# Kernel tuning notes

Measured on AMD Instinct MI355X. Metric: run time of the kernel, lower is better.

Reference implementation:

```python
import jax, jax.numpy as jnp
import numpy as np

NUM_CATEGORIES = 16
INPUT_DIM = 1024
HIDDEN_DIM = 4096
BATCH = 64
SEQ = 256


def setup_inputs() -> dict:
    key = jax.random.key(0)
    k1, k2, k3 = jax.random.split(key, 3)
    x = jax.random.normal(k1, (BATCH, SEQ, INPUT_DIM), dtype=jnp.float32)
    cat_ids = jax.random.randint(k2, (BATCH,), 0, NUM_CATEGORIES, dtype=jnp.int64)
    W = 0.02 * jax.random.normal(k3, (NUM_CATEGORIES, INPUT_DIM, HIDDEN_DIM), dtype=jnp.float32)
    b = jnp.zeros((NUM_CATEGORIES, HIDDEN_DIM), dtype=jnp.float32)
    return {"x": x, "cat_ids": cat_ids, "W": W, "b": b}


def reference(x, cat_ids, W, b):
    # Gather per-sample expert weights then batched matmul, matching torch.bmm semantics.
    selected_W = W[cat_ids]            # [B, input_dim, hidden_dim]
    selected_b = b[cat_ids]            # [B, hidden_dim]
    out = jnp.einsum('bsi,bih->bsh', x, selected_W) + selected_b[:, None, :]
    return out
```

## Files before the change

kernel.cpp:

```cpp
#include <hip/hip_runtime.h>
#include <hip/hip_bf16.h>
#include <stdint.h>

#define BATCH 64
#define SEQ   256
#define KDIM  1024
#define NDIM  4096
#define NCAT  16

#define BM 128
#define BN 128
#define BK 64
#define MT (SEQ/BM)
#define NT (NDIM/BN)
#define TILES_PER_BATCH (MT*NT)
#define NBLOCKS (BATCH*TILES_PER_BATCH)

typedef __attribute__((ext_vector_type(4))) float f32x4;
typedef __attribute__((ext_vector_type(2))) unsigned int u32x2;
typedef __attribute__((ext_vector_type(4))) unsigned int u32x4;
typedef __attribute__((ext_vector_type(8))) short bf16x8;

__device__ __forceinline__ unsigned short f2bf(float f) {
  __hip_bfloat16 h = __float2bfloat16(f);
  return __builtin_bit_cast(unsigned short, h);
}
__device__ __forceinline__ unsigned pack2(float lo, float hi) {
  return (unsigned)f2bf(lo) | ((unsigned)f2bf(hi) << 16);
}

__device__ __forceinline__ void gload16(const void* g, void* l) {
  __builtin_amdgcn_global_load_lds(
      (const __attribute__((address_space(1))) unsigned int*)g,
      (__attribute__((address_space(3))) unsigned int*)l, 16, 0, 0);
}

__global__ void cvt_x_kernel(const float* __restrict__ x,
                             unsigned short* __restrict__ xb, int n8) {
  int i = blockIdx.x * blockDim.x + threadIdx.x;
  const int stride = gridDim.x * blockDim.x;
  for (; i < n8; i += stride) {
    f32x4 a = ((const f32x4*)x)[2 * i];
    f32x4 b = ((const f32x4*)x)[2 * i + 1];
    u32x4 q;
    q[0] = pack2(a[0], a[1]); q[1] = pack2(a[2], a[3]);
    q[2] = pack2(b[0], b[1]); q[3] = pack2(b[2], b[3]);
    ((u32x4*)xb)[i] = q;
  }
}

__global__ void cvt_w_kernel(const float* __restrict__ W,
                             unsigned short* __restrict__ Wt) {
  __shared__ float ls[64][65];
  const int bid = blockIdx.x;
  const int cat = bid >> 10;
  const int rem = bid & 1023;
  const int kt  = rem >> 6;
  const int ntl = rem & 63;
  const int tid = threadIdx.x;

  const float* src = W + (size_t)cat * KDIM * NDIM + (size_t)(kt * 64) * NDIM + ntl * 64;
  const int kl = tid >> 4;
  const int nl = (tid & 15) * 4;
#pragma unroll
  for (int i = 0; i < 4; ++i) {
    f32x4 v = *(const f32x4*)(src + (size_t)(kl + i * 16) * NDIM + nl);
    ls[kl + i * 16][nl + 0] = v[0];
    ls[kl + i * 16][nl + 1] = v[1];
    ls[kl + i * 16][nl + 2] = v[2];
    ls[kl + i * 16][nl + 3] = v[3];
  }
  __syncthreads();
  const int n  = tid >> 2;
  const int k2 = (tid & 3) * 16;
  u32x4 q0, q1;
#pragma unroll
  for (int j = 0; j < 4; ++j) q0[j] = pack2(ls[k2 + 2 * j][n],     ls[k2 + 2 * j + 1][n]);
#pragma unroll
  for (int j = 0; j < 4; ++j) q1[j] = pack2(ls[k2 + 8 + 2 * j][n], ls[k2 + 9 + 2 * j][n]);
  unsigned short* dst = Wt + (size_t)cat * NDIM * KDIM + (size_t)(ntl * 64 + n) * KDIM + kt * 64 + k2;
  *(u32x4*)dst       = q0;
  *(u32x4*)(dst + 8) = q1;
}

__global__ __launch_bounds__(256, 4)
void csl_gemm(const unsigned short* __restrict__ xb,
              const unsigned short* __restrict__ Wt,
              const int*   __restrict__ cat_ids,
              const float* __restrict__ bias,
              float* __restrict__ out)
{
  __shared__ __align__(16) unsigned char sA[BM * BK * 2];
  __shared__ __align__(16) unsigned char sB[BN * BK * 2];
  __shared__ int s_cat[BATCH];

  const int tid  = threadIdx.x;
  const int lane = tid & 63;
  const int wid  = tid >> 6;

  if (tid < BATCH) s_cat[tid] = cat_ids[tid];
  __syncthreads();

  const int bid  = (int)blockIdx.x;
  const int t_id = (bid & 7) * (NBLOCKS / 8) + (bid >> 3);

  const int myc = s_cat[lane];
  int c = 0, base = 0, cc = 0;
  unsigned long long mask = 0ULL;
  for (c = 0; c < NCAT; ++c) {
    mask = __ballot(myc == c);
    cc = __popcll(mask);
    int sz = cc * TILES_PER_BATCH;
    if (t_id < base + sz) break;
    base += sz;
  }
  if (c >= NCAT) return;
  const int idx    = t_id - base;
  const int per_nt = cc * MT;
  const int nt     = idx / per_nt;
  const int r      = idx % per_nt;
  const int want   = r >> 1;
  const int mt     = r & 1;
  unsigned long long mm = mask;
  for (int i = 0; i < want; ++i) mm &= (mm - 1);
  const int batch = __ffsll((long long)mm) - 1;
  const int cat   = c;

  const int m0 = mt * BM;
  const int n0 = nt * BN;

  const size_t xa = ((size_t)batch * SEQ + m0) * KDIM;
  const size_t wa = ((size_t)cat * NDIM + n0) * KDIM;

  const int srow = tid >> 3;
  const int skq  = tid & 7;
  const unsigned ldsb = (unsigned)(wid * 1024);

  f32x4 acc[4][4] = {};
  const int wr   = (wid >> 1) * 64;
  const int wc   = (wid & 1) * 64;
  const int mcol = lane & 15;
  const int kq16 = (lane >> 4) * 16;

  for (int kt = 0; kt < KDIM / BK; ++kt) {
    const int k0 = kt * BK;
    __syncthreads();
#pragma unroll
    for (int s = 0; s < 4; ++s) {
      const unsigned short* gp = xb + xa + (size_t)(s * 32 + srow) * KDIM + (k0 + skq * 8);
      gload16(gp, sA + s * 4096 + ldsb);
    }
#pragma unroll
    for (int s = 0; s < 4; ++s) {
      const unsigned short* gp = Wt + wa + (size_t)(s * 32 + srow) * KDIM + (k0 + skq * 8);
      gload16(gp, sB + s * 4096 + ldsb);
    }
    __syncthreads();
#pragma unroll
    for (int kk = 0; kk < 2; ++kk) {
      const int kb = kk * 64 + kq16;
      bf16x8 af[4], bfr[4];
#pragma unroll
      for (int mi = 0; mi < 4; ++mi)
        af[mi] = *(const bf16x8*)(sA + (unsigned)((wr + mi * 16 + mcol) * 128 + kb));
#pragma unroll
      for (int ni = 0; ni < 4; ++ni)
        bfr[ni] = *(const bf16x8*)(sB + (unsigned)((wc + ni * 16 + mcol) * 128 + kb));
#pragma unroll
      for (int mi = 0; mi < 4; ++mi)
#pragma unroll
        for (int ni = 0; ni < 4; ++ni)
          acc[mi][ni] = __builtin_amdgcn_mfma_f32_16x16x32_bf16(af[mi], bfr[ni], acc[mi][ni], 0, 0, 0);
    }
  }

  const int col_l = lane & 15;
  const int row_l = (lane >> 4) * 4;
#pragma unroll
  for (int mi = 0; mi < 4; ++mi) {
#pragma unroll
    for (int ni = 0; ni < 4; ++ni) {
      int gr = m0 + wr + mi * 16 + row_l;
      int gc = n0 + wc + ni * 16 + col_l;
      float bvl = bias[(size_t)cat * NDIM + gc];
      f32x4 v = acc[mi][ni];
      size_t o = ((size_t)batch * SEQ + gr) * NDIM + gc;
      out[o]            = v[0] + bvl;
      out[o + NDIM]     = v[1] + bvl;
      out[o + 2 * NDIM] = v[2] + bvl;
      out[o + 3 * NDIM] = v[3] + bvl;
    }
  }
}

__global__ __launch_bounds__(256, 2)
void csl_fallback(const float* __restrict__ x,
                  const int*   __restrict__ cat_ids,
                  const float* __restrict__ W,
                  const float* __restrict__ bias,
                  float* __restrict__ out)
{
  __shared__ __align__(16) unsigned char sA[BM * BK * 2];
  __shared__ __align__(16) unsigned char sB[BN * BK * 2];
  __shared__ int s_cat[BATCH];

  const int tid  = threadIdx.x;
  const int lane = tid & 63;
  const int wid  = tid >> 6;

  if (tid < BATCH) s_cat[tid] = cat_ids[tid];
  __syncthreads();

  const int myc = s_cat[lane];
  int t_id = (int)blockIdx.x;
  int c = 0, base = 0, cc = 0;
  unsigned long long mask = 0ULL;
  for (c = 0; c < NCAT; ++c) {
    mask = __ballot(myc == c);
    cc = __popcll(mask);
    int sz = cc * TILES_PER_BATCH;
    if (t_id < base + sz) break;
    base += sz;
  }
  if (c >= NCAT) return;
  const int idx    = t_id - base;
  const int per_nt = cc * MT;
  const int nt     = idx / per_nt;
  const int r      = idx % per_nt;
  const int want   = r >> 1;
  const int mt     = r & 1;
  unsigned long long mm = mask;
  for (int i = 0; i < want; ++i) mm &= (mm - 1);
  const int batch = __ffsll((long long)mm) - 1;
  const int cat   = c;

  const int m0 = mt * BM;
  const int n0 = nt * BN;

  const size_t x_base = ((size_t)batch * SEQ + m0) * KDIM;
  const size_t w_base = (size_t)cat * KDIM * NDIM + n0;

  f32x4 acc[4][4] = {};
  const int wr = (wid >> 1) * 64;
  const int wc = (wid & 1) * 64;

  for (int kt = 0; kt < KDIM / BK; ++kt) {
    const int k0 = kt * BK;
    f32x4 av[4][2];
#pragma unroll
    for (int s = 0; s < 4; ++s) {
      int seg  = tid + s * 256;
      int arow = seg >> 3;
      int ak   = (seg & 7) << 3;
      const float* gp = x + x_base + (size_t)arow * KDIM + (size_t)(k0 + ak);
      av[s][0] = *(const f32x4*)gp;
      av[s][1] = *(const f32x4*)(gp + 4);
    }
    f32x4 bv[2][4];
#pragma unroll
    for (int s = 0; s < 2; ++s) {
      int u  = tid + s * 256;
      int nq = u & 31;
      int kq = u >> 5;
      const float* gp = W + w_base + (size_t)(k0 + kq * 4) * NDIM + (size_t)(nq * 4);
#pragma unroll
      for (int rr = 0; rr < 4; ++rr)
        bv[s][rr] = *(const f32x4*)(gp + (size_t)rr * NDIM);
    }
    __syncthreads();
#pragma unroll
    for (int s = 0; s < 4; ++s) {
      int seg  = tid + s * 256;
      int arow = seg >> 3;
      int akb  = (seg & 7) << 4;
      unsigned byte = (unsigned)(arow * (BK * 2)) + ((unsigned)akb ^ (((unsigned)arow & 7u) << 4));
      u32x4 q;
      q[0] = pack2(av[s][0][0], av[s][0][1]);
      q[1] = pack2(av[s][0][2], av[s][0][3]);
      q[2] = pack2(av[s][1][0], av[s][1][1]);
      q[3] = pack2(av[s][1][2], av[s][1][3]);
      *(u32x4*)(sA + byte) = q;
    }
#pragma unroll
    for (int s = 0; s < 2; ++s) {
      int u  = tid + s * 256;
      int nq = u & 31;
      int kq = u >> 5;
      unsigned swz = ((unsigned)nq & 7u) << 4;
#pragma unroll
      for (int i = 0; i < 4; ++i) {
        int n = nq * 4 + i;
        unsigned byte = (unsigned)(n * (BK * 2)) + (((unsigned)(kq * 8)) ^ swz);
        u32x2 d;
        d[0] = pack2(bv[s][0][i], bv[s][1][i]);
        d[1] = pack2(bv[s][2][i], bv[s][3][i]);
        *(u32x2*)(sB + byte) = d;
      }
    }
    __syncthreads();
#pragma unroll
    for (int kk = 0; kk < 2; ++kk) {
      const int kb = kk * 64 + ((lane >> 4) << 4);
      bf16x8 af[4], bfr[4];
#pragma unroll
      for (int mi = 0; mi < 4; ++mi) {
        int row = wr + mi * 16 + (lane & 15);
        unsigned byte = (unsigned)(row * (BK * 2)) + ((unsigned)kb ^ (((unsigned)row & 7u) << 4));
        af[mi] = *(const bf16x8*)(sA + byte);
      }
#pragma unroll
      for (int ni = 0; ni < 4; ++ni) {
        int n = wc + ni * 16 + (lane & 15);
        unsigned byte = (unsigned)(n * (BK * 2)) + ((unsigned)kb ^ ((((unsigned)n >> 2) & 7u) << 4));
        bfr[ni] = *(const bf16x8*)(sB + byte);
      }
#pragma unroll
      for (int mi = 0; mi < 4; ++mi)
#pragma unroll
        for (int ni = 0; ni < 4; ++ni)
          acc[mi][ni] = __builtin_amdgcn_mfma_f32_16x16x32_bf16(af[mi], bfr[ni], acc[mi][ni], 0, 0, 0);
    }
  }

  const int col_l = lane & 15;
  const int row_l = (lane >> 4) * 4;
#pragma unroll
  for (int mi = 0; mi < 4; ++mi) {
#pragma unroll
    for (int ni = 0; ni < 4; ++ni) {
      int gr = m0 + wr + mi * 16 + row_l;
      int gc = n0 + wc + ni * 16 + col_l;
      float bvl = bias[(size_t)cat * NDIM + gc];
      f32x4 v = acc[mi][ni];
      size_t o = ((size_t)batch * SEQ + gr) * NDIM + gc;
      out[o]            = v[0] + bvl;
      out[o + NDIM]     = v[1] + bvl;
      out[o + 2 * NDIM] = v[2] + bvl;
      out[o + 3 * NDIM] = v[3] + bvl;
    }
  }
}

extern "C" void kernel_launch(void* const* d_in, const int* in_sizes, int n_in,
                              void* d_out, int out_size, void* d_ws, size_t ws_size,
                              hipStream_t stream) {
  const float* x       = (const float*)d_in[0];
  const int*   cat_ids = (const int*)d_in[1];
  const float* W       = (const float*)d_in[2];
  const float* bias    = (const float*)d_in[3];
  float*       out     = (float*)d_out;
  (void)in_sizes; (void)n_in; (void)out_size;

  const size_t wt_elems = (size_t)NCAT * NDIM * KDIM;
  const size_t xb_elems = (size_t)BATCH * SEQ * KDIM;
  const size_t need = (wt_elems + xb_elems) * sizeof(unsigned short);

  if (ws_size >= need) {
    unsigned short* Wt = (unsigned short*)d_ws;
    unsigned short* xb = Wt + wt_elems;
    hipLaunchKernelGGL(cvt_x_kernel, dim3(2048), dim3(256), 0, stream,
                       x, xb, (int)(xb_elems / 8));
    hipLaunchKernelGGL(cvt_w_kernel, dim3(NCAT * (KDIM / 64) * (NDIM / 64)), dim3(256), 0, stream,
                       W, Wt);
    hipLaunchKernelGGL(csl_gemm, dim3(NBLOCKS), dim3(256), 0, stream,
                       xb, Wt, cat_ids, bias, out);
  } else {
    hipLaunchKernelGGL(csl_fallback, dim3(NBLOCKS), dim3(256), 0, stream,
                       x, cat_ids, W, bias, out);
  }
}
```

Baseline: 299.8 us.

## Use 256x256 tiles with double-buffered pre-swizzled LDS pipeline in grouped GEMM

The main GEMM moves from 128x128 tiles with 256 threads to 256x256 tiles with 512 threads. It uses a 128KB double-buffered LDS pipeline that prefetches the next K-tiles while the current one is computed, with explicit barriers, waitcnts and setprio around the MFMA phases. The conversion kernels now write x and W as bf16 tiles already swizzled in the LDS image, so direct global-to-LDS loads avoid bank conflicts and need only contiguous copies. The aim is to raise arithmetic intensity and hide load latency. The cost is fewer blocks (1024), higher register pressure from 32 accumulators, and a more fragile hand-scheduled sync pattern.

```diff
diff --git a/kernel.cpp b/kernel.cpp
--- a/kernel.cpp
+++ b/kernel.cpp
@@ -8,16 +8,14 @@
 #define NDIM  4096
 #define NCAT  16
 
-#define BM 128
-#define BN 128
+#define BM 256
+#define BN 256
 #define BK 64
-#define MT (SEQ/BM)
-#define NT (NDIM/BN)
-#define TILES_PER_BATCH (MT*NT)
-#define NBLOCKS (BATCH*TILES_PER_BATCH)
+#define NT_G (NDIM/BN)
+#define KT_G (KDIM/BK)
+#define GEMM_BLOCKS (BATCH*NT_G)
 
 typedef __attribute__((ext_vector_type(4))) float f32x4;
-typedef __attribute__((ext_vector_type(2))) unsigned int u32x2;
 typedef __attribute__((ext_vector_type(4))) unsigned int u32x4;
 typedef __attribute__((ext_vector_type(8))) short bf16x8;
 
@@ -28,29 +26,37 @@
 __device__ __forceinline__ unsigned pack2(float lo, float hi) {
   return (unsigned)f2bf(lo) | ((unsigned)f2bf(hi) << 16);
 }
-
 __device__ __forceinline__ void gload16(const void* g, void* l) {
   __builtin_amdgcn_global_load_lds(
       (const __attribute__((address_space(1))) unsigned int*)g,
       (__attribute__((address_space(3))) unsigned int*)l, 16, 0, 0);
 }
 
+
 __global__ void cvt_x_kernel(const float* __restrict__ x,
-                             unsigned short* __restrict__ xb, int n8) {
-  int i = blockIdx.x * blockDim.x + threadIdx.x;
-  const int stride = gridDim.x * blockDim.x;
-  for (; i < n8; i += stride) {
-    f32x4 a = ((const f32x4*)x)[2 * i];
-    f32x4 b = ((const f32x4*)x)[2 * i + 1];
-    u32x4 q;
-    q[0] = pack2(a[0], a[1]); q[1] = pack2(a[2], a[3]);
-    q[2] = pack2(b[0], b[1]); q[3] = pack2(b[2], b[3]);
-    ((u32x4*)xb)[i] = q;
-  }
+                             unsigned char* __restrict__ xb_t) {
+  int g = blockIdx.x * 256 + threadIdx.x;
+  const int row = g >> 7;
+  const int c   = g & 127;
+  const int b   = row >> 8;
+  const int s   = row & 255;
+  const int kt  = c >> 3;
+  const int ck  = c & 7;
+  const int h   = s >> 7;
+  const int r   = s & 127;
+  const float* src = x + (size_t)row * KDIM + c * 8;
+  f32x4 a = *(const f32x4*)src;
+  f32x4 d = *(const f32x4*)(src + 4);
+  u32x4 q;
+  q[0] = pack2(a[0], a[1]); q[1] = pack2(a[2], a[3]);
+  q[2] = pack2(d[0], d[1]); q[3] = pack2(d[2], d[3]);
+  unsigned off = (unsigned)(((b * 16 + kt) * 2 + h) * 16384)
+               + (unsigned)(r * 128) + (((unsigned)(ck * 16)) ^ (((unsigned)r & 7u) << 4));
+  *(u32x4*)(xb_t + off) = q;
 }
 
 __global__ void cvt_w_kernel(const float* __restrict__ W,
-                             unsigned short* __restrict__ Wt) {
+                             unsigned char* __restrict__ Wt) {
   __shared__ float ls[64][65];
   const int bid = blockIdx.x;
   const int cat = bid >> 10;
@@ -78,31 +84,39 @@
   for (int j = 0; j < 4; ++j) q0[j] = pack2(ls[k2 + 2 * j][n],     ls[k2 + 2 * j + 1][n]);
 #pragma unroll
   for (int j = 0; j < 4; ++j) q1[j] = pack2(ls[k2 + 8 + 2 * j][n], ls[k2 + 9 + 2 * j][n]);
-  unsigned short* dst = Wt + (size_t)cat * NDIM * KDIM + (size_t)(ntl * 64 + n) * KDIM + kt * 64 + k2;
-  *(u32x4*)dst       = q0;
-  *(u32x4*)(dst + 8) = q1;
-}
-
-__global__ __launch_bounds__(256, 4)
-void csl_gemm(const unsigned short* __restrict__ xb,
-              const unsigned short* __restrict__ Wt,
+
+  const int nt   = ntl >> 2;
+  const int sub  = ntl & 3;
+  const int h    = sub >> 1;
+  const int r    = (sub & 1) * 64 + n;
+  const unsigned sw = ((unsigned)r & 7u) << 4;
+  unsigned base = (unsigned)(cat * 8388608) + (unsigned)(nt * 524288)
+                + (unsigned)((kt * 2 + h) * 16384) + (unsigned)(r * 128);
+  *(u32x4*)(Wt + base + (((unsigned)(k2 * 2))      ^ sw)) = q0;
+  *(u32x4*)(Wt + base + (((unsigned)(k2 * 2 + 16)) ^ sw)) = q1;
+}
+
+__global__ __launch_bounds__(512, 2)
+void csl_gemm(const unsigned char* __restrict__ xb_t,
+              const unsigned char* __restrict__ Wt,
               const int*   __restrict__ cat_ids,
               const float* __restrict__ bias,
               float* __restrict__ out)
 {
-  __shared__ __align__(16) unsigned char sA[BM * BK * 2];
-  __shared__ __align__(16) unsigned char sB[BN * BK * 2];
+  __shared__ __align__(16) unsigned char lds[131072];
   __shared__ int s_cat[BATCH];
 
   const int tid  = threadIdx.x;
   const int lane = tid & 63;
   const int wid  = tid >> 6;
+  const int wm   = wid >> 2;
+  const int wn   = wid & 3;
 
   if (tid < BATCH) s_cat[tid] = cat_ids[tid];
   __syncthreads();
 
   const int bid  = (int)blockIdx.x;
-  const int t_id = (bid & 7) * (NBLOCKS / 8) + (bid >> 3);
+  const int t_id = (bid & 7) * (GEMM_BLOCKS / 8) + (bid >> 3);
 
   const int myc = s_cat[lane];
   int c = 0, base = 0, cc = 0;
@@ -110,13 +124,158 @@
   for (c = 0; c < NCAT; ++c) {
     mask = __ballot(myc == c);
     cc = __popcll(mask);
-    int sz = cc * TILES_PER_BATCH;
+    int sz = cc * NT_G;
     if (t_id < base + sz) break;
     base += sz;
   }
   if (c >= NCAT) return;
+  const int idx = t_id - base;
+  const int nt  = idx / cc;
+  const int pos = idx % cc;
+  unsigned long long mm = mask;
+  for (int i = 0; i < pos; ++i) mm &= (mm - 1);
+  const int batch = __ffsll((long long)mm) - 1;
+  const int cat   = c;
+
+  const unsigned char* Ab = xb_t + (size_t)batch * 524288;
+  const unsigned char* Bb = Wt  + (size_t)cat * 8388608 + (size_t)nt * 524288;
+
+  const unsigned tb16 = (unsigned)(tid * 16);
+
+#define STAGE_A(kt, h)                                                     \
+  {                                                                        \
+    const unsigned char* g = Ab + (unsigned)(((kt) * 2 + (h)) * 16384) + tb16; \
+    unsigned char* l = lds + (((kt) & 1) * 65536) + ((h) * 16384) + tb16;  \
+    gload16(g, l); gload16(g + 8192, l + 8192);                            \
+  }
+#define STAGE_B(kt, h)                                                     \
+  {                                                                        \
+    const unsigned char* g = Bb + (unsigned)(((kt) * 2 + (h)) * 16384) + tb16; \
+    unsigned char* l = lds + (((kt) & 1) * 65536) + 32768 + ((h) * 16384) + tb16; \
+    gload16(g, l); gload16(g + 8192, l + 8192);                            \
+  }
+
+  const int lc       = lane & 15;
+  const unsigned sw  = ((unsigned)lc & 7u) << 4;
+  const unsigned kq16 = (unsigned)((lane >> 4) * 16);
+  const unsigned koff0 = kq16 ^ sw;
+  const unsigned koff1 = (64u + kq16) ^ sw;
+  const unsigned bA = (unsigned)(wm * 16384 + lc * 128);
+  const unsigned bB = 32768u + (unsigned)((wn >> 1) * 16384 + (wn & 1) * 8192 + lc * 128);
+#define KOFF(kk) ((kk) ? koff1 : koff0)
+
+  f32x4 acc[8][4] = {};
+  bf16x8 bfr[4];
+
+#define PHASE(mh, kk, DOB, EXTRA)                                          \
+  {                                                                        \
+    if (DOB) {                                                             \
+      _Pragma("unroll")                                                    \
+      for (int ni = 0; ni < 4; ++ni)                                       \
+        bfr[ni] = *(const bf16x8*)(lds + pb + bB + (unsigned)(ni * 2048) + KOFF(kk)); \
+    }                                                                      \
+    bf16x8 af[4];                                                          \
+    _Pragma("unroll")                                                      \
+    for (int mi = 0; mi < 4; ++mi)                                         \
+      af[mi] = *(const bf16x8*)(lds + pb + bA + (unsigned)((mh) * 8192 + mi * 2048) + KOFF(kk)); \
+    EXTRA                                                                  \
+    __builtin_amdgcn_s_barrier();                                          \
+    asm volatile("s_waitcnt lgkmcnt(0)" ::: "memory");                     \
+    __builtin_amdgcn_sched_barrier(0);                                     \
+    __builtin_amdgcn_s_setprio(1);                                         \
+    _Pragma("unroll")                                                      \
+    for (int mi = 0; mi < 4; ++mi)                                         \
+      _Pragma("unroll")                                                    \
+      for (int ni = 0; ni < 4; ++ni)                                       \
+        acc[(mh) * 4 + mi][ni] = __builtin_amdgcn_mfma_f32_16x16x32_bf16(  \
+            af[mi], bfr[ni], acc[(mh) * 4 + mi][ni], 0, 0, 0);             \
+    __builtin_amdgcn_s_setprio(0);                                         \
+    __builtin_amdgcn_s_barrier();                                          \
+  }
+
+  STAGE_A(0, 0); STAGE_A(0, 1); STAGE_B(0, 0); STAGE_B(0, 1);
+  STAGE_A(1, 0); STAGE_A(1, 1); STAGE_B(1, 0);
+  asm volatile("s_waitcnt vmcnt(6)" ::: "memory");
+  __builtin_amdgcn_s_barrier();
+
+  for (int t = 0; t < KT_G; ++t) {
+    const unsigned pb = (unsigned)((t & 1) * 65536);
+    PHASE(0, 0, 1, { if (t + 1 < KT_G) STAGE_B(t + 1, 1); })
+    PHASE(1, 0, 0, {})
+    PHASE(0, 1, 1, {})
+    PHASE(1, 1, 0, {})
+    if (t + 2 < KT_G) { STAGE_A(t + 2, 0); STAGE_A(t + 2, 1); STAGE_B(t + 2, 0); }
+    if (t < KT_G - 1) {
+      if (t + 2 < KT_G) asm volatile("s_waitcnt vmcnt(6)" ::: "memory");
+      else              asm volatile("s_waitcnt vmcnt(0)" ::: "memory");
+      __builtin_amdgcn_s_barrier();
+    }
+  }
+
+  const int col_l = lane & 15;
+  const int row_l = (lane >> 4) * 4;
+#pragma unroll
+  for (int mf = 0; mf < 8; ++mf) {
+#pragma unroll
+    for (int ni = 0; ni < 4; ++ni) {
+      int gr = wm * 128 + mf * 16 + row_l;
+      int gc = nt * BN + wn * 64 + ni * 16 + col_l;
+      float bvl = bias[(size_t)cat * NDIM + gc];
+      f32x4 v = acc[mf][ni];
+      size_t o = ((size_t)batch * SEQ + gr) * NDIM + gc;
+      out[o]            = v[0] + bvl;
+      out[o + NDIM]     = v[1] + bvl;
+      out[o + 2 * NDIM] = v[2] + bvl;
+      out[o + 3 * NDIM] = v[3] + bvl;
+    }
+  }
+#undef PHASE
+#undef KOFF
+#undef STAGE_A
+#undef STAGE_B
+}
+
+#define FBM 128
+#define FBN 128
+#define FBK 64
+#define FMT (SEQ/FBM)
+#define FNT (NDIM/FBN)
+#define FTPB (FMT*FNT)
+#define FNB (BATCH*FTPB)
+typedef __attribute__((ext_vector_type(2))) unsigned int u32x2;
+
+__global__ __launch_bounds__(256, 2)
+void csl_fallback(const float* __restrict__ x,
+                  const int*   __restrict__ cat_ids,
+                  const float* __restrict__ W,
+                  const float* __restrict__ bias,
+                  float* __restrict__ out)
+{
+  __shared__ __align__(16) unsigned char sA[FBM * FBK * 2];
+  __shared__ __align__(16) unsigned char sB[FBN * FBK * 2];
+  __shared__ int s_cat[BATCH];
+
+  const int tid  = threadIdx.x;
+  const int lane = tid & 63;
+  const int wid  = tid >> 6;
+
+  if (tid < BATCH) s_cat[tid] = cat_ids[tid];
+  __syncthreads();
+
+  const int myc = s_cat[lane];
+  int t_id = (int)blockIdx.x;
+  int c = 0, base = 0, cc = 0;
+  unsigned long long mask = 0ULL;
+  for (c = 0; c < NCAT; ++c) {
+    mask = __ballot(myc == c);
+    cc = __popcll(mask);
+    int sz = cc * FTPB;
+    if (t_id < base + sz) break;
+    base += sz;
+  }
+  if (c >= NCAT) return;
   const int idx    = t_id - base;
-  const int per_nt = cc * MT;
+  const int per_nt = cc * FMT;
   const int nt     = idx / per_nt;
   const int r      = idx % per_nt;
   const int want   = r >> 1;
@@ -126,46 +285,86 @@
   const int batch = __ffsll((long long)mm) - 1;
   const int cat   = c;
 
-  const int m0 = mt * BM;
-  const int n0 = nt * BN;
-
-  const size_t xa = ((size_t)batch * SEQ + m0) * KDIM;
-  const size_t wa = ((size_t)cat * NDIM + n0) * KDIM;
-
-  const int srow = tid >> 3;
-  const int skq  = tid & 7;
-  const unsigned ldsb = (unsigned)(wid * 1024);
+  const int m0 = mt * FBM;
+  const int n0 = nt * FBN;
+
+  const size_t x_base = ((size_t)batch * SEQ + m0) * KDIM;
+  const size_t w_base = (size_t)cat * KDIM * NDIM + n0;
 
   f32x4 acc[4][4] = {};
-  const int wr   = (wid >> 1) * 64;
-  const int wc   = (wid & 1) * 64;
-  const int mcol = lane & 15;
-  const int kq16 = (lane >> 4) * 16;
-
-  for (int kt = 0; kt < KDIM / BK; ++kt) {
-    const int k0 = kt * BK;
+  const int wr = (wid >> 1) * 64;
+  const int wc = (wid & 1) * 64;
+
+  for (int kt = 0; kt < KDIM / FBK; ++kt) {
+    const int k0 = kt * FBK;
+    f32x4 av[4][2];
+#pragma unroll
+    for (int s = 0; s < 4; ++s) {
+      int seg  = tid + s * 256;
+      int arow = seg >> 3;
+      int ak   = (seg & 7) << 3;
+      const float* gp = x + x_base + (size_t)arow * KDIM + (size_t)(k0 + ak);
+      av[s][0] = *(const f32x4*)gp;
+      av[s][1] = *(const f32x4*)(gp + 4);
+    }
+    f32x4 bv[2][4];
+#pragma unroll
+    for (int s = 0; s < 2; ++s) {
+      int u  = tid + s * 256;
+      int nq = u & 31;
+      int kq = u >> 5;
+      const float* gp = W + w_base + (size_t)(k0 + kq * 4) * NDIM + (size_t)(nq * 4);
+#pragma unroll
+      for (int rr = 0; rr < 4; ++rr)
+        bv[s][rr] = *(const f32x4*)(gp + (size_t)rr * NDIM);
+    }
     __syncthreads();
 #pragma unroll
     for (int s = 0; s < 4; ++s) {
-      const unsigned short* gp = xb + xa + (size_t)(s * 32 + srow) * KDIM + (k0 + skq * 8);
-      gload16(gp, sA + s * 4096 + ldsb);
-    }
-#pragma unroll
-    for (int s = 0; s < 4; ++s) {
-      const unsigned short* gp = Wt + wa + (size_t)(s * 32 + srow) * KDIM + (k0 + skq * 8);
-      gload16(gp, sB + s * 4096 + ldsb);
+      int seg  = tid + s * 256;
+      int arow = seg >> 3;
+      int akb  = (seg & 7) << 4;
+      unsigned byte = (unsigned)(arow * (FBK * 2)) + ((unsigned)akb ^ (((unsigned)arow & 7u) << 4));
+      u32x4 q;
+      q[0] = pack2(av[s][0][0], av[s][0][1]);
+      q[1] = pack2(av[s][0][2], av[s][0][3]);
+      q[2] = pack2(av[s][1][0], av[s][1][1]);
+      q[3] = pack2(av[s][1][2], av[s][1][3]);
+      *(u32x4*)(sA + byte) = q;
+    }
+#pragma unroll
+    for (int s = 0; s < 2; ++s) {
+      int u  = tid + s * 256;
+      int nq = u & 31;
+      int kq = u >> 5;
+      unsigned swz = ((unsigned)nq & 7u) << 4;
+#pragma unroll
+      for (int i = 0; i < 4; ++i) {
+        int n = nq * 4 + i;
+        unsigned byte = (unsigned)(n * (FBK * 2)) + (((unsigned)(kq * 8)) ^ swz);
+        u32x2 d;
+        d[0] = pack2(bv[s][0][i], bv[s][1][i]);
+        d[1] = pack2(bv[s][2][i], bv[s][3][i]);
+        *(u32x2*)(sB + byte) = d;
+      }
     }
     __syncthreads();
 #pragma unroll
     for (int kk = 0; kk < 2; ++kk) {
-      const int kb = kk * 64 + kq16;
+      const int kb = kk * 64 + ((lane >> 4) << 4);
       bf16x8 af[4], bfr[4];
 #pragma unroll
-      for (int mi = 0; mi < 4; ++mi)
-        af[mi] = *(const bf16x8*)(sA + (unsigned)((wr + mi * 16 + mcol) * 128 + kb));
-#pragma unroll
-      for (int ni = 0; ni < 4; ++ni)
-        bfr[ni] = *(const bf16x8*)(sB + (unsigned)((wc + ni * 16 + mcol) * 128 + kb));
+      for (int mi = 0; mi < 4; ++mi) {
+        int row = wr + mi * 16 + (lane & 15);
+        unsigned byte = (unsigned)(row * (FBK * 2)) + ((unsigned)kb ^ (((unsigned)row & 7u) << 4));
+        af[mi] = *(const bf16x8*)(sA + byte);
+      }
+#pragma unroll
+      for (int ni = 0; ni < 4; ++ni) {
+        int n = wc + ni * 16 + (lane & 15);
+        unsigned byte = (unsigned)(n * (FBK * 2)) + ((unsigned)kb ^ ((((unsigned)n >> 2) & 7u) << 4));
+        bfr[ni] = *(const bf16x8*)(sB + byte);
+      }
 #pragma unroll
       for (int mi = 0; mi < 4; ++mi)
 #pragma unroll
@@ -193,154 +392,6 @@
   }
 }
 
-__global__ __launch_bounds__(256, 2)
-void csl_fallback(const float* __restrict__ x,
-                  const int*   __restrict__ cat_ids,
-                  const float* __restrict__ W,
-                  const float* __restrict__ bias,
-                  float* __restrict__ out)
-{
-  __shared__ __align__(16) unsigned char sA[BM * BK * 2];
-  __shared__ __align__(16) unsigned char sB[BN * BK * 2];
-  __shared__ int s_cat[BATCH];
-
-  const int tid  = threadIdx.x;
-  const int lane = tid & 63;
-  const int wid  = tid >> 6;
-
-  if (tid < BATCH) s_cat[tid] = cat_ids[tid];
-  __syncthreads();
-
-  const int myc = s_cat[lane];
-  int t_id = (int)blockIdx.x;
-  int c = 0, base = 0, cc = 0;
-  unsigned long long mask = 0ULL;
-  for (c = 0; c < NCAT; ++c) {
-    mask = __ballot(myc == c);
-    cc = __popcll(mask);
-    int sz = cc * TILES_PER_BATCH;
-    if (t_id < base + sz) break;
-    base += sz;
-  }
-  if (c >= NCAT) return;
-  const int idx    = t_id - base;
-  const int per_nt = cc * MT;
-  const int nt     = idx / per_nt;
-  const int r      = idx % per_nt;
-  const int want   = r >> 1;
-  const int mt     = r & 1;
-  unsigned long long mm = mask;
-  for (int i = 0; i < want; ++i) mm &= (mm - 1);
-  const int batch = __ffsll((long long)mm) - 1;
-  const int cat   = c;
-
-  const int m0 = mt * BM;
-  const int n0 = nt * BN;
-
-  const size_t x_base = ((size_t)batch * SEQ + m0) * KDIM;
-  const size_t w_base = (size_t)cat * KDIM * NDIM + n0;
-
-  f32x4 acc[4][4] = {};
-  const int wr = (wid >> 1) * 64;
-  const int wc = (wid & 1) * 64;
-
-  for (int kt = 0; kt < KDIM / BK; ++kt) {
-    const int k0 = kt * BK;
-    f32x4 av[4][2];
-#pragma unroll
-    for (int s = 0; s < 4; ++s) {
-      int seg  = tid + s * 256;
-      int arow = seg >> 3;
-      int ak   = (seg & 7) << 3;
-      const float* gp = x + x_base + (size_t)arow * KDIM + (size_t)(k0 + ak);
-      av[s][0] = *(const f32x4*)gp;
-      av[s][1] = *(const f32x4*)(gp + 4);
-    }
-    f32x4 bv[2][4];
-#pragma unroll
-    for (int s = 0; s < 2; ++s) {
-      int u  = tid + s * 256;
-      int nq = u & 31;
-      int kq = u >> 5;
-      const float* gp = W + w_base + (size_t)(k0 + kq * 4) * NDIM + (size_t)(nq * 4);
-#pragma unroll
-      for (int rr = 0; rr < 4; ++rr)
-        bv[s][rr] = *(const f32x4*)(gp + (size_t)rr * NDIM);
-    }
-    __syncthreads();
-#pragma unroll
-    for (int s = 0; s < 4; ++s) {
-      int seg  = tid + s * 256;
-      int arow = seg >> 3;
-      int akb  = (seg & 7) << 4;
-      unsigned byte = (unsigned)(arow * (BK * 2)) + ((unsigned)akb ^ (((unsigned)arow & 7u) << 4));
-      u32x4 q;
-      q[0] = pack2(av[s][0][0], av[s][0][1]);
-      q[1] = pack2(av[s][0][2], av[s][0][3]);
-      q[2] = pack2(av[s][1][0], av[s][1][1]);
-      q[3] = pack2(av[s][1][2], av[s][1][3]);
-      *(u32x4*)(sA + byte) = q;
-    }
-#pragma unroll
-    for (int s = 0; s < 2; ++s) {
-      int u  = tid + s * 256;
-      int nq = u & 31;
-      int kq = u >> 5;
-      unsigned swz = ((unsigned)nq & 7u) << 4;
-#pragma unroll
-      for (int i = 0; i < 4; ++i) {
-        int n = nq * 4 + i;
-        unsigned byte = (unsigned)(n * (BK * 2)) + (((unsigned)(kq * 8)) ^ swz);
-        u32x2 d;
-        d[0] = pack2(bv[s][0][i], bv[s][1][i]);
-        d[1] = pack2(bv[s][2][i], bv[s][3][i]);
-        *(u32x2*)(sB + byte) = d;
-      }
-    }
-    __syncthreads();
-#pragma unroll
-    for (int kk = 0; kk < 2; ++kk) {
-      const int kb = kk * 64 + ((lane >> 4) << 4);
-      bf16x8 af[4], bfr[4];
-#pragma unroll
-      for (int mi = 0; mi < 4; ++mi) {
-        int row = wr + mi * 16 + (lane & 15);
-        unsigned byte = (unsigned)(row * (BK * 2)) + ((unsigned)kb ^ (((unsigned)row & 7u) << 4));
-        af[mi] = *(const bf16x8*)(sA + byte);
-      }
-#pragma unroll
-      for (int ni = 0; ni < 4; ++ni) {
-        int n = wc + ni * 16 + (lane & 15);
-        unsigned byte = (unsigned)(n * (BK * 2)) + ((unsigned)kb ^ ((((unsigned)n >> 2) & 7u) << 4));
-        bfr[ni] = *(const bf16x8*)(sB + byte);
-      }
-#pragma unroll
-      for (int mi = 0; mi < 4; ++mi)
-#pragma unroll
-        for (int ni = 0; ni < 4; ++ni)
-          acc[mi][ni] = __builtin_amdgcn_mfma_f32_16x16x32_bf16(af[mi], bfr[ni], acc[mi][ni], 0, 0, 0);
-    }
-  }
-
-  const int col_l = lane & 15;
-  const int row_l = (lane >> 4) * 4;
-#pragma unroll
-  for (int mi = 0; mi < 4; ++mi) {
-#pragma unroll
-    for (int ni = 0; ni < 4; ++ni) {
-      int gr = m0 + wr + mi * 16 + row_l;
-      int gc = n0 + wc + ni * 16 + col_l;
-      float bvl = bias[(size_t)cat * NDIM + gc];
-      f32x4 v = acc[mi][ni];
-      size_t o = ((size_t)batch * SEQ + gr) * NDIM + gc;
-      out[o]            = v[0] + bvl;
-      out[o + NDIM]     = v[1] + bvl;
-      out[o + 2 * NDIM] = v[2] + bvl;
-      out[o + 3 * NDIM] = v[3] + bvl;
-    }
-  }
-}
-
 extern "C" void kernel_launch(void* const* d_in, const int* in_sizes, int n_in,
                               void* d_out, int out_size, void* d_ws, size_t ws_size,
                               hipStream_t stream) {
@@ -351,21 +402,21 @@
   float*       out     = (float*)d_out;
   (void)in_sizes; (void)n_in; (void)out_size;
 
-  const size_t wt_elems = (size_t)NCAT * NDIM * KDIM;
-  const size_t xb_elems = (size_t)BATCH * SEQ * KDIM;
-  const size_t need = (wt_elems + xb_elems) * sizeof(unsigned short);
+  const size_t wt_bytes = (size_t)NCAT * NDIM * KDIM * 2;
+  const size_t xb_bytes = (size_t)BATCH * SEQ * KDIM * 2;
+  const size_t need = wt_bytes + xb_bytes;
 
   if (ws_size >= need) {
-    unsigned short* Wt = (unsigned short*)d_ws;
-    unsigned short* xb = Wt + wt_elems;
-    hipLaunchKernelGGL(cvt_x_kernel, dim3(2048), dim3(256), 0, stream,
-                       x, xb, (int)(xb_elems / 8));
+    unsigned char* Wt   = (unsigned char*)d_ws;
+    unsigned char* xb_t = Wt + wt_bytes;
+    hipLaunchKernelGGL(cvt_x_kernel, dim3((BATCH * SEQ * KDIM / 8) / 256), dim3(256), 0, stream,
+                       x, xb_t);
     hipLaunchKernelGGL(cvt_w_kernel, dim3(NCAT * (KDIM / 64) * (NDIM / 64)), dim3(256), 0, stream,
                        W, Wt);
-    hipLaunchKernelGGL(csl_gemm, dim3(NBLOCKS), dim3(256), 0, stream,
-                       xb, Wt, cat_ids, bias, out);
+    hipLaunchKernelGGL(csl_gemm, dim3(GEMM_BLOCKS), dim3(512), 0, stream,
+                       xb_t, Wt, cat_ids, bias, out);
   } else {
-    hipLaunchKernelGGL(csl_fallback, dim3(NBLOCKS), dim3(256), 0, stream,
+    hipLaunchKernelGGL(csl_fallback, dim3(FNB), dim3(256), 0, stream,
                        x, cat_ids, W, bias, out);
   }
 }
```

New measurement: 322.2 us. +7.5%, slower.

## Pre-tile and XOR-swizzle bf16 operands, fuse conversion kernels into one launch

Applied to the files above, without the earlier changes.

The x and W conversion kernels become a single launch, and both now write bf16 data straight into a tiled layout. Each 128x64 tile is contiguous and XOR-swizzled by row, so the GEMM can fill LDS with fully contiguous 16-byte loads and read MFMA fragments without bank conflicts. The layout change removes strided global loads and LDS bank conflicts, and the fusion removes one kernel launch. Launch bounds drop from 4 to 2 waves per SIMD, which gives more registers but may lower occupancy.

```diff
diff --git a/kernel.cpp b/kernel.cpp
--- a/kernel.cpp
+++ b/kernel.cpp
@@ -17,7 +17,6 @@
 #define NBLOCKS (BATCH*TILES_PER_BATCH)
 
 typedef __attribute__((ext_vector_type(4))) float f32x4;
-typedef __attribute__((ext_vector_type(2))) unsigned int u32x2;
 typedef __attribute__((ext_vector_type(4))) unsigned int u32x4;
 typedef __attribute__((ext_vector_type(8))) short bf16x8;
 
@@ -28,64 +27,84 @@
 __device__ __forceinline__ unsigned pack2(float lo, float hi) {
   return (unsigned)f2bf(lo) | ((unsigned)f2bf(hi) << 16);
 }
-
 __device__ __forceinline__ void gload16(const void* g, void* l) {
   __builtin_amdgcn_global_load_lds(
       (const __attribute__((address_space(1))) unsigned int*)g,
       (__attribute__((address_space(3))) unsigned int*)l, 16, 0, 0);
 }
 
-__global__ void cvt_x_kernel(const float* __restrict__ x,
-                             unsigned short* __restrict__ xb, int n8) {
-  int i = blockIdx.x * blockDim.x + threadIdx.x;
-  const int stride = gridDim.x * blockDim.x;
-  for (; i < n8; i += stride) {
-    f32x4 a = ((const f32x4*)x)[2 * i];
-    f32x4 b = ((const f32x4*)x)[2 * i + 1];
+
+#define CVT_W_BLOCKS (NCAT*(KDIM/64)*(NDIM/64))
+#define CVT_X_BLOCKS ((BATCH*SEQ*KDIM/8)/256)
+
+__global__ void cvt_fused(const float* __restrict__ x,
+                          const float* __restrict__ W,
+                          unsigned char* __restrict__ xb_t,
+                          unsigned char* __restrict__ Wt) {
+  __shared__ float ls[64][65];
+  const int tid = threadIdx.x;
+
+  if (blockIdx.x < CVT_W_BLOCKS) {
+    const int bid = blockIdx.x;
+    const int cat = bid >> 10;
+    const int rem = bid & 1023;
+    const int kt  = rem >> 6;
+    const int ntl = rem & 63;
+
+    const float* src = W + (size_t)cat * KDIM * NDIM + (size_t)(kt * 64) * NDIM + ntl * 64;
+    const int kl = tid >> 4;
+    const int nl = (tid & 15) * 4;
+#pragma unroll
+    for (int i = 0; i < 4; ++i) {
+      f32x4 v = *(const f32x4*)(src + (size_t)(kl + i * 16) * NDIM + nl);
+      ls[kl + i * 16][nl + 0] = v[0];
+      ls[kl + i * 16][nl + 1] = v[1];
+      ls[kl + i * 16][nl + 2] = v[2];
+      ls[kl + i * 16][nl + 3] = v[3];
+    }
+    __syncthreads();
+    const int n  = tid >> 2;
+    const int k2 = (tid & 3) * 16;
+    u32x4 q0, q1;
+#pragma unroll
+    for (int j = 0; j < 4; ++j) q0[j] = pack2(ls[k2 + 2 * j][n],     ls[k2 + 2 * j + 1][n]);
+#pragma unroll
+    for (int j = 0; j < 4; ++j) q1[j] = pack2(ls[k2 + 8 + 2 * j][n], ls[k2 + 9 + 2 * j][n]);
+
+    const int nt   = ntl >> 2;
+    const int sub  = ntl & 3;
+    const int h    = sub >> 1;
+    const int r    = (sub & 1) * 64 + n;
+    const unsigned sw = ((unsigned)r & 7u) << 4;
+    unsigned base = (unsigned)(cat * 8388608) + (unsigned)(nt * 524288)
+                  + (unsigned)((kt * 2 + h) * 16384) + (unsigned)(r * 128);
+    *(u32x4*)(Wt + base + (((unsigned)(k2 * 2))      ^ sw)) = q0;
+    *(u32x4*)(Wt + base + (((unsigned)(k2 * 2 + 16)) ^ sw)) = q1;
+  } else {
+    int g = (blockIdx.x - CVT_W_BLOCKS) * 256 + tid;
+    const int row = g >> 7;
+    const int c   = g & 127;
+    const int b   = row >> 8;
+    const int s   = row & 255;
+    const int kt  = c >> 3;
+    const int ck  = c & 7;
+    const int h   = s >> 7;
+    const int r   = s & 127;
+    const float* src = x + (size_t)row * KDIM + c * 8;
+    f32x4 a = *(const f32x4*)src;
+    f32x4 d = *(const f32x4*)(src + 4);
     u32x4 q;
     q[0] = pack2(a[0], a[1]); q[1] = pack2(a[2], a[3]);
-    q[2] = pack2(b[0], b[1]); q[3] = pack2(b[2], b[3]);
-    ((u32x4*)xb)[i] = q;
-  }
-}
-
-__global__ void cvt_w_kernel(const float* __restrict__ W,
-                             unsigned short* __restrict__ Wt) {
-  __shared__ float ls[64][65];
-  const int bid = blockIdx.x;
-  const int cat = bid >> 10;
-  const int rem = bid & 1023;
-  const int kt  = rem >> 6;
-  const int ntl = rem & 63;
-  const int tid = threadIdx.x;
-
-  const float* src = W + (size_t)cat * KDIM * NDIM + (size_t)(kt * 64) * NDIM + ntl * 64;
-  const int kl = tid >> 4;
-  const int nl = (tid & 15) * 4;
-#pragma unroll
-  for (int i = 0; i < 4; ++i) {
-    f32x4 v = *(const f32x4*)(src + (size_t)(kl + i * 16) * NDIM + nl);
-    ls[kl + i * 16][nl + 0] = v[0];
-    ls[kl + i * 16][nl + 1] = v[1];
-    ls[kl + i * 16][nl + 2] = v[2];
-    ls[kl + i * 16][nl + 3] = v[3];
-  }
-  __syncthreads();
-  const int n  = tid >> 2;
-  const int k2 = (tid & 3) * 16;
-  u32x4 q0, q1;
-#pragma unroll
-  for (int j = 0; j < 4; ++j) q0[j] = pack2(ls[k2 + 2 * j][n],     ls[k2 + 2 * j + 1][n]);
-#pragma unroll
-  for (int j = 0; j < 4; ++j) q1[j] = pack2(ls[k2 + 8 + 2 * j][n], ls[k2 + 9 + 2 * j][n]);
-  unsigned short* dst = Wt + (size_t)cat * NDIM * KDIM + (size_t)(ntl * 64 + n) * KDIM + kt * 64 + k2;
-  *(u32x4*)dst       = q0;
-  *(u32x4*)(dst + 8) = q1;
-}
-
-__global__ __launch_bounds__(256, 4)
-void csl_gemm(const unsigned short* __restrict__ xb,
-              const unsigned short* __restrict__ Wt,
+    q[2] = pack2(d[0], d[1]); q[3] = pack2(d[2], d[3]);
+    unsigned off = (unsigned)(((b * 16 + kt) * 2 + h) * 16384)
+                 + (unsigned)(r * 128) + (((unsigned)(ck * 16)) ^ (((unsigned)r & 7u) << 4));
+    *(u32x4*)(xb_t + off) = q;
+  }
+}
+
+__global__ __launch_bounds__(256, 2)
+void csl_gemm(const unsigned char* __restrict__ xb_t,
+              const unsigned char* __restrict__ Wt,
               const int*   __restrict__ cat_ids,
               const float* __restrict__ bias,
               float* __restrict__ out)
@@ -129,43 +148,44 @@
   const int m0 = mt * BM;
   const int n0 = nt * BN;
 
-  const size_t xa = ((size_t)batch * SEQ + m0) * KDIM;
-  const size_t wa = ((size_t)cat * NDIM + n0) * KDIM;
-
-  const int srow = tid >> 3;
-  const int skq  = tid & 7;
-  const unsigned ldsb = (unsigned)(wid * 1024);
+  const unsigned char* Ab = xb_t + (size_t)batch * 524288 + (unsigned)(mt * 16384);
+  const unsigned char* Bb = Wt + (size_t)cat * 8388608 + (size_t)(nt >> 1) * 524288
+                          + (unsigned)((nt & 1) * 16384);
+
+  const unsigned tb16 = (unsigned)(tid * 16);
+
+  const int lc        = lane & 15;
+  const unsigned sw   = ((unsigned)lc & 7u) << 4;
+  const unsigned kq16 = (unsigned)((lane >> 4) * 16);
+  const unsigned koff0 = kq16 ^ sw;
+  const unsigned koff1 = (64u + kq16) ^ sw;
 
   f32x4 acc[4][4] = {};
-  const int wr   = (wid >> 1) * 64;
-  const int wc   = (wid & 1) * 64;
-  const int mcol = lane & 15;
-  const int kq16 = (lane >> 4) * 16;
+  const int wr = (wid >> 1) * 64;
+  const int wc = (wid & 1) * 64;
+  const unsigned rowA = (unsigned)((wr + lc) * 128);
+  const unsigned rowB = (unsigned)((wc + lc) * 128);
 
   for (int kt = 0; kt < KDIM / BK; ++kt) {
-    const int k0 = kt * BK;
-    __syncthreads();
-#pragma unroll
-    for (int s = 0; s < 4; ++s) {
-      const unsigned short* gp = xb + xa + (size_t)(s * 32 + srow) * KDIM + (k0 + skq * 8);
-      gload16(gp, sA + s * 4096 + ldsb);
-    }
-#pragma unroll
-    for (int s = 0; s < 4; ++s) {
-      const unsigned short* gp = Wt + wa + (size_t)(s * 32 + srow) * KDIM + (k0 + skq * 8);
-      gload16(gp, sB + s * 4096 + ldsb);
-    }
+    const unsigned ko = (unsigned)(kt * 32768);
+    __syncthreads();
+#pragma unroll
+    for (int s = 0; s < 4; ++s)
+      gload16(Ab + ko + (unsigned)(s * 4096) + tb16, sA + s * 4096 + tb16);
+#pragma unroll
+    for (int s = 0; s < 4; ++s)
+      gload16(Bb + ko + (unsigned)(s * 4096) + tb16, sB + s * 4096 + tb16);
     __syncthreads();
 #pragma unroll
     for (int kk = 0; kk < 2; ++kk) {
-      const int kb = kk * 64 + kq16;
+      const unsigned koff = kk ? koff1 : koff0;
       bf16x8 af[4], bfr[4];
 #pragma unroll
       for (int mi = 0; mi < 4; ++mi)
-        af[mi] = *(const bf16x8*)(sA + (unsigned)((wr + mi * 16 + mcol) * 128 + kb));
+        af[mi] = *(const bf16x8*)(sA + rowA + (unsigned)(mi * 2048) + koff);
 #pragma unroll
       for (int ni = 0; ni < 4; ++ni)
-        bfr[ni] = *(const bf16x8*)(sB + (unsigned)((wc + ni * 16 + mcol) * 128 + kb));
+        bfr[ni] = *(const bf16x8*)(sB + rowB + (unsigned)(ni * 2048) + koff);
 #pragma unroll
       for (int mi = 0; mi < 4; ++mi)
 #pragma unroll
@@ -192,6 +212,8 @@
     }
   }
 }
+
+typedef __attribute__((ext_vector_type(2))) unsigned int u32x2;
 
 __global__ __launch_bounds__(256, 2)
 void csl_fallback(const float* __restrict__ x,
@@ -351,19 +373,17 @@
   float*       out     = (float*)d_out;
   (void)in_sizes; (void)n_in; (void)out_size;
 
-  const size_t wt_elems = (size_t)NCAT * NDIM * KDIM;
-  const size_t xb_elems = (size_t)BATCH * SEQ * KDIM;
-  const size_t need = (wt_elems + xb_elems) * sizeof(unsigned short);
+  const size_t wt_bytes = (size_t)NCAT * NDIM * KDIM * 2;
+  const size_t xb_bytes = (size_t)BATCH * SEQ * KDIM * 2;
+  const size_t need = wt_bytes + xb_bytes;
 
   if (ws_size >= need) {
-    unsigned short* Wt = (unsigned short*)d_ws;
-    unsigned short* xb = Wt + wt_elems;
-    hipLaunchKernelGGL(cvt_x_kernel, dim3(2048), dim3(256), 0, stream,
-                       x, xb, (int)(xb_elems / 8));
-    hipLaunchKernelGGL(cvt_w_kernel, dim3(NCAT * (KDIM / 64) * (NDIM / 64)), dim3(256), 0, stream,
-                       W, Wt);
+    unsigned char* Wt   = (unsigned char*)d_ws;
+    unsigned char* xb_t = Wt + wt_bytes;
+    hipLaunchKernelGGL(cvt_fused, dim3(CVT_W_BLOCKS + CVT_X_BLOCKS), dim3(256), 0, stream,
+                       x, W, xb_t, Wt);
     hipLaunchKernelGGL(csl_gemm, dim3(NBLOCKS), dim3(256), 0, stream,
-                       xb, Wt, cat_ids, bias, out);
+                       xb_t, Wt, cat_ids, bias, out);
   } else {
     hipLaunchKernelGGL(csl_fallback, dim3(NBLOCKS), dim3(256), 0, stream,
                        x, cat_ids, W, bias, out);
```

New measurement: 280.7 us. 6.4% less time.
